# Optimization experiments

Hardware: AMD Instinct MI355X
Metric: run time of the kernel (lower is better)

## Reference

```python
import jax, jax.numpy as jnp
import numpy as np

B, N, DIM, H, DH, K = 4, 2048, 512, 6, 64, 16
KEEP_PROB = 0.9  # 1 - dropout_rate
LOG2PI = float(np.log(2.0 * np.pi))
LOG_PRIOR = float(np.log(1.0 / K))


def setup_inputs() -> dict:
    key = jax.random.key(0)
    ks = jax.random.split(key, 7)
    inputs_q = jax.random.normal(ks[0], (B, N, DIM), dtype=jnp.float32)
    # decoder-style causal mask, shape [B, 1, q_len, kv_len]
    causal = jnp.tril(jnp.ones((N, N), dtype=jnp.float32))
    mask = jnp.broadcast_to(causal[None, None], (B, 1, N, N))
    # dropout keep mask broadcast across the query dim: [B, H, 1, kv_len]
    keep = jax.random.bernoulli(ks[1], KEEP_PROB, (B, H, 1, N)).astype(jnp.float32)
    w_qkv = jax.random.normal(ks[2], (DIM, 3 * H * DH), dtype=jnp.float32) * 0.02
    w_out = jax.random.normal(ks[3], (H * DH, DIM), dtype=jnp.float32) * 0.02
    mu_lookup = jax.random.normal(ks[4], (K, DIM), dtype=jnp.float32)
    logvar_lookup = jax.random.normal(ks[5], (K, DIM), dtype=jnp.float32) * 0.1
    return {
        "inputs_q": inputs_q,
        "mask": mask,
        "keep": keep,
        "w_qkv": w_qkv,
        "w_out": w_out,
        "mu_lookup": mu_lookup,
        "logvar_lookup": logvar_lookup,
    }


def reference(inputs_q, mask, keep, w_qkv, w_out, mu_lookup, logvar_lookup):
    # --- MultiHeadDotProductAttention (self-attn path) ---
    qkv = (inputs_q @ w_qkv).reshape(B, N, 3, H, DH)  # [B,N,3,H,DH]
    q, k, v = qkv[:, :, 0], qkv[:, :, 1], qkv[:, :, 2]
    # bias: 0 where mask > 0, -1e10 elsewhere (note: no 1/sqrt(d) scaling, as in source)
    bias = jnp.where(mask > 0, 0.0, -1e10)
    attn_weights = jnp.einsum('bqhd,bkhd->bhqk', q, k) + bias  # [B,H,N,N]
    attn_weights = jax.nn.softmax(attn_weights, axis=-1)
    # broadcast dropout: mask shared across the query dim
    attn_weights = attn_weights * keep / KEEP_PROB
    attn_out = jnp.einsum('bhqk,bkhd->bqhd', attn_weights, v)
    attn_out = attn_out.reshape(B, N, H * DH) @ w_out  # [B,N,DIM]

    # --- GMM posterior approx q(y|x) ~= p(y|z) (approx_qy_x, vectorized over k) ---
    z = attn_out.mean(axis=1)  # pooled latent, [B,DIM]
    diff = z[:, None, :] - mu_lookup[None]  # [B,K,DIM]
    llh = -0.5 * jnp.sum(
        diff * diff / jnp.exp(logvar_lookup)[None] + logvar_lookup[None] + LOG2PI,
        axis=-1,
    )  # [B,K]
    logLogit_qy_x = llh + LOG_PRIOR
    qy_x = jax.nn.softmax(logLogit_qy_x, axis=1)  # [B,K]

    # combine mixture mean back in so both branches are live in one output
    return attn_out + (qy_x @ mu_lookup)[:, None, :]
```

## Files before the change

### kernel.cpp

```cpp
#include <hip/hip_runtime.h>
#include <cstdint>
#include <cstddef>

#define NH 6
#define NSEQ 2048
#define DIMD 512
#define BATCH 4
#define HD 384
#define LOG2PI_F 1.8378770664093453f
#define LOG2E_F 1.4426950408889634f
#define M12L2_F (-17.312340490667562f)

typedef __attribute__((ext_vector_type(8))) short short8;
typedef __attribute__((ext_vector_type(8))) unsigned short ushort8;
typedef __attribute__((ext_vector_type(4))) unsigned short ushort4v;
typedef __attribute__((ext_vector_type(4))) float floatx4;

__device__ inline unsigned short f2bf(float f){
  unsigned int u = __float_as_uint(f);
  u += 0x7FFFu + ((u>>16)&1u);
  return (unsigned short)(u>>16);
}

#define GLD16(gp, lp) __builtin_amdgcn_global_load_lds( \
  (const __attribute__((address_space(1))) void*)(gp), \
  (__attribute__((address_space(3))) void*)(lp), 16, 0, 0)

__global__ __launch_bounds__(256) void convert_x(
    const float* __restrict__ xq, unsigned short* __restrict__ xbf)
{
  int i = blockIdx.x*256 + threadIdx.x;
  floatx4 v = *(const floatx4*)(xq + (size_t)i*4);
  ushort4v r;
  #pragma unroll
  for(int j=0;j<4;j++) r[j] = f2bf(v[j]);
  *(ushort4v*)(xbf + (size_t)i*4) = r;
}

__global__ __launch_bounds__(256) void wtrans(
    const float* __restrict__ src, unsigned short* __restrict__ dst, int R, int C)
{
  __shared__ __attribute__((aligned(16))) unsigned short Ls[64*72];
  const int t = threadIdx.x;
  const int r = t>>2, c0 = (t&3)*16;
  const int d0 = blockIdx.y*64, n0 = blockIdx.x*64;
  #pragma unroll
  for (int j=0;j<16;j+=4){
    floatx4 v = *(const floatx4*)(src + (size_t)(d0+r)*C + n0 + c0 + j);
    #pragma unroll
    for(int jj=0;jj<4;jj++) Ls[r*72 + c0+j+jj] = f2bf(v[jj]);
  }
  __syncthreads();
  #pragma unroll
  for (int j=0;j<16;j+=8){
    ushort8 o;
    #pragma unroll
    for(int jj=0;jj<8;jj++) o[jj] = Ls[(c0+j+jj)*72 + r];
    *(ushort8*)(dst + (size_t)(n0+r)*R + d0 + c0 + j) = o;
  }
}

__global__ __launch_bounds__(256) void gemm_qkv(
    const unsigned short* __restrict__ A,
    const unsigned short* __restrict__ Bt,
    const float* __restrict__ keep,
    unsigned short* __restrict__ Qo, unsigned short* __restrict__ Ko,
    unsigned short* __restrict__ Vt)
{
  __shared__ __attribute__((aligned(16))) unsigned short Cs[128*132];
  unsigned short* As = Cs;
  unsigned short* Bs = Cs + 128*64;
  const int tid = threadIdx.x;
  const int w = tid>>6, lane = tid&63;
  const int wr = w>>1, wc = w&1;
  const int quad = lane>>4, l16 = lane&15;
  const int tM = blockIdx.x*128, tN = blockIdx.y*128;
  const int r8 = lane>>3, c8 = (lane&7)*8;
  floatx4 acc[4][4];
  floatx4 zed = {0.f,0.f,0.f,0.f};
  #pragma unroll
  for (int i=0;i<4;i++)
    #pragma unroll
    for(int j=0;j<4;j++) acc[i][j] = zed;

  for (int k0=0; k0<512; k0+=64){
    #pragma unroll
    for (int i=0;i<4;i++){
      int row = w*32 + i*8;
      GLD16(A  + (size_t)(tM+row+r8)*512 + k0 + c8, As + row*64);
      GLD16(Bt + (size_t)(tN+row+r8)*512 + k0 + c8, Bs + row*64);
    }
    __syncthreads();
    #pragma unroll
    for (int kk=0; kk<64; kk+=32){
      short8 af[4], bf[4];
      #pragma unroll
      for(int mt=0;mt<4;mt++)
        af[mt] = *(const short8*)(As + (wr*64+mt*16+l16)*64 + kk + quad*8);
      #pragma unroll
      for(int nt=0;nt<4;nt++)
        bf[nt] = *(const short8*)(Bs + (wc*64+nt*16+l16)*64 + kk + quad*8);
      #pragma unroll
      for(int mt=0;mt<4;mt++)
        #pragma unroll
        for(int nt=0;nt<4;nt++)
          acc[mt][nt] = __builtin_amdgcn_mfma_f32_16x16x32_bf16(af[mt], bf[nt], acc[mt][nt], 0,0,0);
    }
    __syncthreads();
  }
  #pragma unroll
  for(int mt=0;mt<4;mt++)
    #pragma unroll
    for(int nt=0;nt<4;nt++){
      int gcol = tN + wc*64 + nt*16 + l16;
      float qs = (gcol < 384) ? LOG2E_F : 1.0f;
      #pragma unroll
      for(int r=0;r<4;r++)
        Cs[(wr*64+mt*16+quad*4+r)*132 + wc*64+nt*16+l16] = f2bf(acc[mt][nt][r]*qs);
    }
  __syncthreads();
  if (blockIdx.y < 6){
    const int row = tid>>1, colh = (tid&1)*64;
    const int gcol0 = tN + colh;
    const int t = gcol0/384, rem = gcol0 - t*384, h = rem>>6;
    const int grow = tM + row, b = grow>>11, n = grow & 2047;
    unsigned short* dst = (t==0 ? Qo : Ko) + ((size_t)((b*NH+h)*NSEQ+n))*64;
    #pragma unroll
    for(int j=0;j<8;j++)
      *(ushort8*)(dst + j*8) = *(const ushort8*)(Cs + row*132 + colh + j*8);
  } else {
    const int dcol = tid>>1;
    const int nh   = (tid&1)*64;
    const int gcol = tN + dcol;
    const int rem = gcol - 768, h = rem>>6, dh = rem&63;
    const int b = tM>>11, nb = tM & 2047;
    const float* kp = keep + (size_t)(b*NH+h)*NSEQ + nb + nh;
    unsigned short* dst = Vt + ((size_t)((b*NH+h)*64 + dh))*NSEQ + nb + nh;
    #pragma unroll
    for (int j8=0;j8<8;j8++){
      floatx4 k0 = *(const floatx4*)(kp + j8*8);
      floatx4 k1 = *(const floatx4*)(kp + j8*8 + 4);
      ushort8 o;
      #pragma unroll
      for(int u=0;u<4;u++)
        o[u]   = (k0[u] < 0.5f) ? (unsigned short)0 : Cs[(nh + j8*8 + u)*132 + dcol];
      #pragma unroll
      for(int u=0;u<4;u++)
        o[4+u] = (k1[u] < 0.5f) ? (unsigned short)0 : Cs[(nh + j8*8 + 4 + u)*132 + dcol];
      *(ushort8*)(dst + j8*8) = o;
    }
  }
}

__global__ __launch_bounds__(256, 4) void attn_kernel(
    const unsigned short* __restrict__ Qg, const unsigned short* __restrict__ Kg,
    const unsigned short* __restrict__ VtG,
    unsigned short* __restrict__ atp)
{
  __shared__ __attribute__((aligned(16))) char sm[4*32*68*4 + 4*32*4];
  const int tid = threadIdx.x;
  const int w = tid>>6, lane = tid&63;
  unsigned short* Ps = (unsigned short*)sm + w*(32*72);
  float* Oc   = (float*)sm;
  float* accs = (float*)(sm + 4*32*68*4);
  const int quad = lane>>4, l16 = lane&15;
  const int bid = blockIdx.x;
  const int idx = bid>>3;
  const int bh  = (bid&7) + 8*(idx % 3);
  const int c   = 63 - idx/3;
  const int b = bh/NH, h = bh - b*NH;
  const unsigned short* Qb = Qg  + (size_t)bh*NSEQ*64;
  const unsigned short* Kb = Kg  + (size_t)bh*NSEQ*64;
  const unsigned short* Vb = VtG + (size_t)bh*64*NSEQ;
  const int q0 = c*32;
  const int nkt = (c>>1) + 1;

  short8 qf[2][2];
  #pragma unroll
  for(int mt=0;mt<2;mt++)
    #pragma unroll
    for(int kc=0;kc<2;kc++)
      qf[mt][kc] = *(const short8*)(Qb + (size_t)(q0+mt*16+l16)*64 + kc*32 + quad*8);

  short8 onesf;
  #pragma unroll
  for(int j=0;j<8;j++) onesf[j] = (short)0x3F80;

  floatx4 O[2][4];
  floatx4 accl[2];
  floatx4 zed = {0.f,0.f,0.f,0.f};
  #pragma unroll
  for(int mt=0;mt<2;mt++){
    #pragma unroll
    for(int dt=0;dt<4;dt++) O[mt][dt] = zed;
    accl[mt] = zed;
  }

  for (int kt = w; kt < nkt; kt += 4){
    const int kB = kt*64;
    short8 vf[2][4];
    const unsigned short* vp0 = Vb + kB;
    #pragma unroll
    for(int kh=0;kh<2;kh++)
      #pragma unroll
      for(int dt=0;dt<4;dt++)
        vf[kh][dt] = *(const short8*)(vp0 + (size_t)(dt*16+l16)*NSEQ + kh*32 + quad*8);

    floatx4 sacc[2][4];
    floatx4 m12 = {M12L2_F, M12L2_F, M12L2_F, M12L2_F};
    #pragma unroll
    for(int mt=0;mt<2;mt++)
      #pragma unroll
      for(int nt=0;nt<4;nt++) sacc[mt][nt] = m12;
    const unsigned short* kp0 = Kb + (size_t)kB*64;
    #pragma unroll
    for(int nt=0;nt<4;nt++){
      short8 kf0 = *(const short8*)(kp0 + (size_t)(nt*16+l16)*64 + quad*8);
      short8 kf1 = *(const short8*)(kp0 + (size_t)(nt*16+l16)*64 + 32 + quad*8);
      #pragma unroll
      for(int mt=0;mt<2;mt++){
        sacc[mt][nt] = __builtin_amdgcn_mfma_f32_16x16x32_bf16(qf[mt][0], kf0, sacc[mt][nt], 0,0,0);
        sacc[mt][nt] = __builtin_amdgcn_mfma_f32_16x16x32_bf16(qf[mt][1], kf1, sacc[mt][nt], 0,0,0);
      }
    }

    const bool dia = (kt == nkt-1);
    #pragma unroll
    for(int mt=0;mt<2;mt++){
      #pragma unroll
      for(int nt=0;nt<4;nt++){
        int key = kB + nt*16 + l16;
        #pragma unroll
        for(int r=0;r<4;r++){
          float p = exp2f(sacc[mt][nt][r]);
          if (dia) p = (key <= q0 + mt*16 + quad*4 + r) ? p : 0.f;
          Ps[(mt*16+quad*4+r)*72 + nt*16 + l16] = f2bf(p);
        }
      }
    }
    #pragma unroll
    for(int kh=0;kh<2;kh++){
      #pragma unroll
      for(int mt=0;mt<2;mt++){
        short8 pf = *(const short8*)(Ps + (mt*16+l16)*72 + kh*32 + quad*8);
        accl[mt] = __builtin_amdgcn_mfma_f32_16x16x32_bf16(pf, onesf, accl[mt], 0,0,0);
        #pragma unroll
        for(int dt=0;dt<4;dt++)
          O[mt][dt] = __builtin_amdgcn_mfma_f32_16x16x32_bf16(pf, vf[kh][dt], O[mt][dt], 0,0,0);
      }
    }
  }

  __syncthreads();
  {
    float* Ow = Oc + w*(32*68);
    #pragma unroll
    for(int mt=0;mt<2;mt++){
      #pragma unroll
      for(int dt=0;dt<4;dt++)
        #pragma unroll
        for(int r=0;r<4;r++)
          Ow[(mt*16+quad*4+r)*68 + dt*16 + l16] = O[mt][dt][r];
      if (l16 == 0){
        #pragma unroll
        for(int r=0;r<4;r++)
          accs[w*32 + mt*16+quad*4+r] = accl[mt][r];
      }
    }
  }
  __syncthreads();

  const int orow = tid>>3, oc0 = (tid&7)*8;
  float as = accs[0*32+orow] + accs[1*32+orow] + accs[2*32+orow] + accs[3*32+orow];
  float sc2 = (1.0f/0.9f) / as;
  float vsum[8];
  #pragma unroll
  for(int j=0;j<8;j++) vsum[j] = 0.f;
  #pragma unroll
  for(int s=0;s<4;s++){
    const float* p = Oc + s*(32*68) + orow*68 + oc0;
    #pragma unroll
    for(int j=0;j<8;j++) vsum[j] += p[j];
  }
  ushort8 o;
  #pragma unroll
  for(int j=0;j<8;j++) o[j] = f2bf(vsum[j]*sc2);
  unsigned short* dstp = atp + ((size_t)(b*NSEQ + q0 + orow))*HD + h*64 + oc0;
  *(ushort8*)dstp = o;
}

__global__ __launch_bounds__(256) void gemm_proj(
    const unsigned short* __restrict__ A,
    const unsigned short* __restrict__ Bt,
    float* __restrict__ out,
    float* __restrict__ z)
{
  __shared__ __attribute__((aligned(16))) unsigned short As[128*64];
  __shared__ __attribute__((aligned(16))) unsigned short Bs[128*64];
  const int tid = threadIdx.x;
  const int w = tid>>6, lane = tid&63;
  const int wr = w>>1, wc = w&1;
  const int quad = lane>>4, l16 = lane&15;
  const int tM = blockIdx.x*128, tN = blockIdx.y*128;
  const int r8 = lane>>3, c8 = (lane&7)*8;
  floatx4 acc[4][4];
  floatx4 zed = {0.f,0.f,0.f,0.f};
  #pragma unroll
  for (int i=0;i<4;i++)
    #pragma unroll
    for(int j=0;j<4;j++) acc[i][j] = zed;

  for (int k0=0; k0<384; k0+=64){
    #pragma unroll
    for (int i=0;i<4;i++){
      int row = w*32 + i*8;
      GLD16(A  + (size_t)(tM+row+r8)*384 + k0 + c8, As + row*64);
      GLD16(Bt + (size_t)(tN+row+r8)*384 + k0 + c8, Bs + row*64);
    }
    __syncthreads();
    #pragma unroll
    for (int kk=0; kk<64; kk+=32){
      short8 af[4], bf[4];
      #pragma unroll
      for(int mt=0;mt<4;mt++)
        af[mt] = *(const short8*)(As + (wr*64+mt*16+l16)*64 + kk + quad*8);
      #pragma unroll
      for(int nt=0;nt<4;nt++)
        bf[nt] = *(const short8*)(Bs + (wc*64+nt*16+l16)*64 + kk + quad*8);
      #pragma unroll
      for(int mt=0;mt<4;mt++)
        #pragma unroll
        for(int nt=0;nt<4;nt++)
          acc[mt][nt] = __builtin_amdgcn_mfma_f32_16x16x32_bf16(af[mt], bf[nt], acc[mt][nt], 0,0,0);
    }
    __syncthreads();
  }
  #pragma unroll
  for(int mt=0;mt<4;mt++){
    int grow = tM + wr*64 + mt*16 + quad*4;
    #pragma unroll
    for(int nt=0;nt<4;nt++){
      int gcol = tN + wc*64 + nt*16 + l16;
      #pragma unroll
      for(int r=0;r<4;r++)
        out[(size_t)(grow+r)*512 + gcol] = acc[mt][nt][r];
    }
  }
  #pragma unroll
  for(int nt=0;nt<4;nt++){
    float s = 0.f;
    #pragma unroll
    for(int mt=0;mt<4;mt++)
      #pragma unroll
      for(int r=0;r<4;r++) s += acc[mt][nt][r];
    s += __shfl_xor(s, 16, 64);
    s += __shfl_xor(s, 32, 64);
    if (quad == 0){
      int gcol = tN + wc*64 + nt*16 + l16;
      atomicAdd(&z[(tM>>11)*DIMD + gcol], s);
    }
  }
}

__global__ __launch_bounds__(256) void gmm_kernel(
    const float* __restrict__ z, const float* __restrict__ mu,
    const float* __restrict__ lv, float* __restrict__ c)
{
  __shared__ float sh[16];
  __shared__ float qy[16];
  int tid = threadIdx.x;
  int k = tid>>4, li = tid&15;
  int b = blockIdx.x;
  float part = 0.f;
  for(int d=li; d<DIMD; d+=16){
    float zz = z[b*DIMD+d] * (1.0f/2048.0f);
    float m = mu[k*DIMD+d], l = lv[k*DIMD+d];
    float diff = zz - m;
    part += diff*diff*__expf(-l) + l + LOG2PI_F;
  }
  #pragma unroll
  for(int off=8;off>=1;off>>=1) part += __shfl_xor(part, off, 64);
  if (li==0) sh[k] = part;
  __syncthreads();
  if (tid<16){
    float logit = -0.5f*sh[tid];
    float mx = logit;
    #pragma unroll
    for(int off=8;off>=1;off>>=1) mx = fmaxf(mx, __shfl_xor(mx, off, 64));
    float e = __expf(logit-mx);
    float se = e;
    #pragma unroll
    for(int off=8;off>=1;off>>=1) se += __shfl_xor(se, off, 64);
    qy[tid] = e/se;
  }
  __syncthreads();
  for(int d=tid; d<DIMD; d+=256){
    float accv = 0.f;
    #pragma unroll
    for(int kk=0;kk<16;kk++) accv += qy[kk]*mu[kk*DIMD+d];
    c[b*DIMD+d] = accv;
  }
}

__global__ __launch_bounds__(256) void final_add(
    float* __restrict__ out, const float* __restrict__ c)
{
  size_t i = ((size_t)blockIdx.x*256 + threadIdx.x)*4;
  int d = (int)(i & 511);
  int b = (int)(i >> 20);
  floatx4 a = *(const floatx4*)(out + i);
  floatx4 cc = *(const floatx4*)(c + b*DIMD + d);
  *(floatx4*)(out + i) = a + cc;
}

extern "C" void kernel_launch(void* const* d_in, const int* in_sizes, int n_in,
                              void* d_out, int out_size, void* d_ws, size_t ws_size,
                              hipStream_t stream) {
  const float* inputs_q = (const float*)d_in[0];
  const float* keep  = (const float*)d_in[2];
  const float* w_qkv = (const float*)d_in[3];
  const float* w_out = (const float*)d_in[4];
  const float* mu    = (const float*)d_in[5];
  const float* lv    = (const float*)d_in[6];
  float* out = (float*)d_out;
  char* ws = (char*)d_ws;
  size_t off = 0;
  auto alloc = [&](size_t bytes){ void* p = ws + off; off += (bytes + 255) & ~(size_t)255; return p; };
  unsigned short* Qb  = (unsigned short*)alloc((size_t)24*2048*64*2);
  unsigned short* Kb  = (unsigned short*)alloc((size_t)24*2048*64*2);
  unsigned short* Vt  = (unsigned short*)alloc((size_t)24*64*2048*2);
  unsigned short* xbf = (unsigned short*)alloc((size_t)8192*512*2);
  unsigned short* wqT = (unsigned short*)alloc((size_t)1152*512*2);
  unsigned short* woT = (unsigned short*)alloc((size_t)512*384*2);
  unsigned short* atp = (unsigned short*)alloc((size_t)8192*384*2);
  float* z  = (float*)alloc((size_t)4*512*4);
  float* c  = (float*)alloc((size_t)4*512*4);

  hipMemsetAsync(z, 0, 4*512*4, stream);
  convert_x<<<4096, 256, 0, stream>>>(inputs_q, xbf);
  wtrans<<<dim3(18,8), 256, 0, stream>>>(w_qkv, wqT, 512, 1152);
  wtrans<<<dim3(8,6),  256, 0, stream>>>(w_out, woT, 384, 512);
  gemm_qkv<<<dim3(64,9), 256, 0, stream>>>(xbf, wqT, keep, Qb, Kb, Vt);
  attn_kernel<<<1536, 256, 0, stream>>>(Qb, Kb, Vt, atp);
  gemm_proj<<<dim3(64,4), 256, 0, stream>>>(atp, woT, out, z);
  gmm_kernel<<<4, 256, 0, stream>>>(z, mu, lv, c);
  final_add<<<4096, 256, 0, stream>>>(out, c);
}
```

Measured before the change: 241.7 us.

## Merge prep kernels, swap QK MFMA operands for packed bf16 P stores

Folds the x conversion and both weight transposes into one prep kernel, which removes two launches. In the attention kernel the QK^T MFMA operands are swapped, so each lane holds four consecutive keys for one query row. Those four P values are packed with v_cvt_pk_bf16_f32 and written as one 8-byte LDS store instead of four scalar 2-byte stores. It also precomputes per-lane base pointers and lowers the launch_bounds occupancy hint from 4 to 3, which gives the compiler more registers at the cost of fewer resident waves.

```diff
diff --git a/kernel.cpp b/kernel.cpp
--- a/kernel.cpp
+++ b/kernel.cpp
@@ -15,6 +15,7 @@
 typedef __attribute__((ext_vector_type(8))) unsigned short ushort8;
 typedef __attribute__((ext_vector_type(4))) unsigned short ushort4v;
 typedef __attribute__((ext_vector_type(4))) float floatx4;
+typedef __attribute__((ext_vector_type(2))) unsigned int uint2v;
 
 __device__ inline unsigned short f2bf(float f){
   unsigned int u = __float_as_uint(f);
@@ -26,24 +27,12 @@
   (const __attribute__((address_space(1))) void*)(gp), \
   (__attribute__((address_space(3))) void*)(lp), 16, 0, 0)
 
-__global__ __launch_bounds__(256) void convert_x(
-    const float* __restrict__ xq, unsigned short* __restrict__ xbf)
-{
-  int i = blockIdx.x*256 + threadIdx.x;
-  floatx4 v = *(const floatx4*)(xq + (size_t)i*4);
-  ushort4v r;
-  #pragma unroll
-  for(int j=0;j<4;j++) r[j] = f2bf(v[j]);
-  *(ushort4v*)(xbf + (size_t)i*4) = r;
-}
-
-__global__ __launch_bounds__(256) void wtrans(
-    const float* __restrict__ src, unsigned short* __restrict__ dst, int R, int C)
-{
-  __shared__ __attribute__((aligned(16))) unsigned short Ls[64*72];
-  const int t = threadIdx.x;
+__device__ inline void wtrans_body(
+    const float* __restrict__ src, unsigned short* __restrict__ dst,
+    int R, int C, int bx, int by, unsigned short* Ls, int t)
+{
   const int r = t>>2, c0 = (t&3)*16;
-  const int d0 = blockIdx.y*64, n0 = blockIdx.x*64;
+  const int d0 = by*64, n0 = bx*64;
   #pragma unroll
   for (int j=0;j<16;j+=4){
     floatx4 v = *(const floatx4*)(src + (size_t)(d0+r)*C + n0 + c0 + j);
@@ -57,6 +46,29 @@
     #pragma unroll
     for(int jj=0;jj<8;jj++) o[jj] = Ls[(c0+j+jj)*72 + r];
     *(ushort8*)(dst + (size_t)(n0+r)*R + d0 + c0 + j) = o;
+  }
+}
+
+__global__ __launch_bounds__(256) void prep(
+    const float* __restrict__ xq, unsigned short* __restrict__ xbf,
+    const float* __restrict__ w_qkv, unsigned short* __restrict__ wqT,
+    const float* __restrict__ w_out, unsigned short* __restrict__ woT)
+{
+  __shared__ __attribute__((aligned(16))) unsigned short Ls[64*72];
+  const int bid = blockIdx.x, t = threadIdx.x;
+  if (bid < 4096){
+    int i = bid*256 + t;
+    floatx4 v = *(const floatx4*)(xq + (size_t)i*4);
+    ushort4v r;
+    #pragma unroll
+    for(int j=0;j<4;j++) r[j] = f2bf(v[j]);
+    *(ushort4v*)(xbf + (size_t)i*4) = r;
+  } else if (bid < 4240){
+    int rb = bid - 4096;
+    wtrans_body(w_qkv, wqT, 512, 1152, rb%18, rb/18, Ls, t);
+  } else {
+    int rb = bid - 4240;
+    wtrans_body(w_out, woT, 384, 512, rb%8, rb/8, Ls, t);
   }
 }
 
@@ -152,7 +164,7 @@
   }
 }
 
-__global__ __launch_bounds__(256, 4) void attn_kernel(
+__global__ __launch_bounds__(256, 3) void attn_kernel(
     const unsigned short* __restrict__ Qg, const unsigned short* __restrict__ Kg,
     const unsigned short* __restrict__ VtG,
     unsigned short* __restrict__ atp)
@@ -170,10 +182,14 @@
   const int c   = 63 - idx/3;
   const int b = bh/NH, h = bh - b*NH;
   const unsigned short* Qb = Qg  + (size_t)bh*NSEQ*64;
-  const unsigned short* Kb = Kg  + (size_t)bh*NSEQ*64;
-  const unsigned short* Vb = VtG + (size_t)bh*64*NSEQ;
   const int q0 = c*32;
   const int nkt = (c>>1) + 1;
+  const int q_abs0 = q0 + l16;
+
+  const unsigned short* Kl = Kg  + (size_t)bh*NSEQ*64 + (size_t)l16*64 + quad*8;
+  const unsigned short* Vl = VtG + (size_t)bh*64*NSEQ + (size_t)l16*NSEQ + quad*8;
+  unsigned short* Psw = Ps + l16*72 + quad*4;
+  const unsigned short* Psr = Ps + l16*72 + quad*8;
 
   short8 qf[2][2];
   #pragma unroll
@@ -189,6 +205,7 @@
   floatx4 O[2][4];
   floatx4 accl[2];
   floatx4 zed = {0.f,0.f,0.f,0.f};
+  floatx4 m12v = {M12L2_F, M12L2_F, M12L2_F, M12L2_F};
   #pragma unroll
   for(int mt=0;mt<2;mt++){
     #pragma unroll
@@ -199,50 +216,59 @@
   for (int kt = w; kt < nkt; kt += 4){
     const int kB = kt*64;
     short8 vf[2][4];
-    const unsigned short* vp0 = Vb + kB;
+    const unsigned short* vp0 = Vl + kB;
     #pragma unroll
     for(int kh=0;kh<2;kh++)
       #pragma unroll
       for(int dt=0;dt<4;dt++)
-        vf[kh][dt] = *(const short8*)(vp0 + (size_t)(dt*16+l16)*NSEQ + kh*32 + quad*8);
+        vf[kh][dt] = *(const short8*)(vp0 + (size_t)dt*32768 + kh*32);
 
     floatx4 sacc[2][4];
-    floatx4 m12 = {M12L2_F, M12L2_F, M12L2_F, M12L2_F};
     #pragma unroll
     for(int mt=0;mt<2;mt++)
       #pragma unroll
-      for(int nt=0;nt<4;nt++) sacc[mt][nt] = m12;
-    const unsigned short* kp0 = Kb + (size_t)kB*64;
+      for(int nt=0;nt<4;nt++) sacc[mt][nt] = m12v;
+    const unsigned short* kp0 = Kl + (size_t)kt*4096;
     #pragma unroll
     for(int nt=0;nt<4;nt++){
-      short8 kf0 = *(const short8*)(kp0 + (size_t)(nt*16+l16)*64 + quad*8);
-      short8 kf1 = *(const short8*)(kp0 + (size_t)(nt*16+l16)*64 + 32 + quad*8);
+      short8 kf0 = *(const short8*)(kp0 + nt*1024);
+      short8 kf1 = *(const short8*)(kp0 + nt*1024 + 32);
       #pragma unroll
       for(int mt=0;mt<2;mt++){
-        sacc[mt][nt] = __builtin_amdgcn_mfma_f32_16x16x32_bf16(qf[mt][0], kf0, sacc[mt][nt], 0,0,0);
-        sacc[mt][nt] = __builtin_amdgcn_mfma_f32_16x16x32_bf16(qf[mt][1], kf1, sacc[mt][nt], 0,0,0);
+        sacc[mt][nt] = __builtin_amdgcn_mfma_f32_16x16x32_bf16(kf0, qf[mt][0], sacc[mt][nt], 0,0,0);
+        sacc[mt][nt] = __builtin_amdgcn_mfma_f32_16x16x32_bf16(kf1, qf[mt][1], sacc[mt][nt], 0,0,0);
       }
     }
 
     const bool dia = (kt == nkt-1);
     #pragma unroll
     for(int mt=0;mt<2;mt++){
+      const int qa = q_abs0 + mt*16;
       #pragma unroll
       for(int nt=0;nt<4;nt++){
-        int key = kB + nt*16 + l16;
-        #pragma unroll
-        for(int r=0;r<4;r++){
-          float p = exp2f(sacc[mt][nt][r]);
-          if (dia) p = (key <= q0 + mt*16 + quad*4 + r) ? p : 0.f;
-          Ps[(mt*16+quad*4+r)*72 + nt*16 + l16] = f2bf(p);
+        const int key0 = kB + nt*16 + quad*4;
+        float p0 = exp2f(sacc[mt][nt][0]);
+        float p1 = exp2f(sacc[mt][nt][1]);
+        float p2 = exp2f(sacc[mt][nt][2]);
+        float p3 = exp2f(sacc[mt][nt][3]);
+        if (dia){
+          p0 = (key0   <= qa) ? p0 : 0.f;
+          p1 = (key0+1 <= qa) ? p1 : 0.f;
+          p2 = (key0+2 <= qa) ? p2 : 0.f;
+          p3 = (key0+3 <= qa) ? p3 : 0.f;
         }
+        unsigned int lo, hi;
+        asm("v_cvt_pk_bf16_f32 %0, %1, %2" : "=v"(lo) : "v"(p0), "v"(p1));
+        asm("v_cvt_pk_bf16_f32 %0, %1, %2" : "=v"(hi) : "v"(p2), "v"(p3));
+        uint2v pk; pk[0] = lo; pk[1] = hi;
+        *(uint2v*)(Psw + mt*1152 + nt*16) = pk;
       }
     }
     #pragma unroll
     for(int kh=0;kh<2;kh++){
       #pragma unroll
       for(int mt=0;mt<2;mt++){
-        short8 pf = *(const short8*)(Ps + (mt*16+l16)*72 + kh*32 + quad*8);
+        short8 pf = *(const short8*)(Psr + mt*1152 + kh*32);
         accl[mt] = __builtin_amdgcn_mfma_f32_16x16x32_bf16(pf, onesf, accl[mt], 0,0,0);
         #pragma unroll
         for(int dt=0;dt<4;dt++)
@@ -437,9 +463,7 @@
   float* c  = (float*)alloc((size_t)4*512*4);
 
   hipMemsetAsync(z, 0, 4*512*4, stream);
-  convert_x<<<4096, 256, 0, stream>>>(inputs_q, xbf);
-  wtrans<<<dim3(18,8), 256, 0, stream>>>(w_qkv, wqT, 512, 1152);
-  wtrans<<<dim3(8,6),  256, 0, stream>>>(w_out, woT, 384, 512);
+  prep<<<4288, 256, 0, stream>>>(inputs_q, xbf, w_qkv, wqT, w_out, woT);
   gemm_qkv<<<dim3(64,9), 256, 0, stream>>>(xbf, wqT, keep, Qb, Kb, Vt);
   attn_kernel<<<1536, 256, 0, stream>>>(Qb, Kb, Vt, atp);
   gemm_proj<<<dim3(64,4), 256, 0, stream>>>(atp, woT, out, z);
```

Measured after the change: 234.7 us. 2.9% less time.
